# Optimization experiments

Hardware: AMD Instinct MI355X
Metric: run time of the kernel (lower is better)

The kernel has to match this reference:

```python
import jax, jax.numpy as jnp
import numpy as np

N_NODES = 50000
N_EDGES = 800000
N_GRAPHS = 128
F_IN = 36
HEADS1 = 10
OUT_DIM = 128


def _gat_layer(x, src, dst, W, a_src, a_dst, b, heads, out_c):
    # x: [N, Fin]; W: [Fin, heads*out_c]; a_src/a_dst: [heads, out_c]; b: [heads*out_c]
    N = x.shape[0]
    h = (x @ W).reshape(N, heads, out_c)                      # [N,H,C]
    al_s = jnp.einsum('nhc,hc->nh', h, a_src)                 # [N,H]
    al_d = jnp.einsum('nhc,hc->nh', h, a_dst)                 # [N,H]
    e = jax.nn.leaky_relu(al_s[src] + al_d[dst], negative_slope=0.2)  # [E,H]
    # segment-softmax over incoming edges of each dst node
    m = jax.ops.segment_max(e, dst, num_segments=N)
    m = jnp.where(jnp.isfinite(m), m, 0.0)
    p = jnp.exp(e - m[dst])
    s = jax.ops.segment_sum(p, dst, num_segments=N)
    alpha = p / (s[dst] + 1e-16)                              # [E,H]
    out = jax.ops.segment_sum(alpha[:, :, None] * h[src], dst, num_segments=N)  # [N,H,C]
    return out.reshape(N, heads * out_c) + b


def setup_inputs() -> dict:
    key = jax.random.key(0)
    ks = jax.random.split(key, 12)
    x = jax.random.normal(ks[0], (N_NODES, F_IN), dtype=jnp.float32)
    edge_index = jax.random.randint(ks[1], (2, N_EDGES), 0, N_NODES, dtype=jnp.int64)
    batch = jnp.sort(jax.random.randint(ks[2], (N_NODES,), 0, N_GRAPHS, dtype=jnp.int64))
    g = 0.1  # glorot-ish scale
    W1 = jax.random.normal(ks[3], (F_IN, HEADS1 * F_IN), dtype=jnp.float32) * g
    att_src1 = jax.random.normal(ks[4], (HEADS1, F_IN), dtype=jnp.float32) * g
    att_dst1 = jax.random.normal(ks[5], (HEADS1, F_IN), dtype=jnp.float32) * g
    b1 = jnp.zeros((HEADS1 * F_IN,), dtype=jnp.float32)
    W2 = jax.random.normal(ks[6], (HEADS1 * F_IN, OUT_DIM), dtype=jnp.float32) * g
    att_src2 = jax.random.normal(ks[7], (1, OUT_DIM), dtype=jnp.float32) * g
    att_dst2 = jax.random.normal(ks[8], (1, OUT_DIM), dtype=jnp.float32) * g
    b2 = jnp.zeros((OUT_DIM,), dtype=jnp.float32)
    fc_w = jax.random.normal(ks[9], (OUT_DIM, OUT_DIM), dtype=jnp.float32) * g
    fc_b = jnp.zeros((OUT_DIM,), dtype=jnp.float32)
    return {"x": x, "edge_index": edge_index, "batch": batch,
            "W1": W1, "att_src1": att_src1, "att_dst1": att_dst1, "b1": b1,
            "W2": W2, "att_src2": att_src2, "att_dst2": att_dst2, "b2": b2,
            "fc_w": fc_w, "fc_b": fc_b}


def reference(x, edge_index, batch, W1, att_src1, att_dst1, b1,
              W2, att_src2, att_dst2, b2, fc_w, fc_b):
    N = x.shape[0]
    # PyG GATConv adds self loops by default
    loops = jnp.arange(N, dtype=edge_index.dtype)
    src = jnp.concatenate([edge_index[0], loops])
    dst = jnp.concatenate([edge_index[1], loops])
    # eval mode: dropouts are identity
    h = jax.nn.elu(_gat_layer(x, src, dst, W1, att_src1, att_dst1, b1, HEADS1, F_IN))
    h = _gat_layer(h, src, dst, W2, att_src2, att_dst2, b2, 1, OUT_DIM)
    h = jax.nn.relu(h)
    # global max pool over graphs
    g = jax.ops.segment_max(h, batch, num_segments=N_GRAPHS)
    g = jnp.where(jnp.isfinite(g), g, 0.0)
    out = jax.nn.relu(g @ fc_w + fc_b)
    return out
```

## Files before the change

kernel.cpp:

```cpp
#include <hip/hip_runtime.h>
#include <hip/hip_fp16.h>
#include <math.h>

#define N_NODES  50000
#define N_EDGES  800000
#define E_TOT    850000
#define N_GRAPHS 128
#define F_IN     36
#define NH1      10
#define C1       36
#define D1       360
#define D2       128
#define XW       18

#define SCHUNK  512
#define NCHUNK  98

typedef unsigned int u32;

#if defined(__has_builtin)
#if __has_builtin(__builtin_amdgcn_fdot2)
#define HAVE_FDOT2 1
#endif
#endif
#ifndef HAVE_FDOT2
#define HAVE_FDOT2 0
#endif

typedef _Float16 h2v __attribute__((ext_vector_type(2)));

static __device__ __forceinline__ float2 h2f(u32 u) {
  __half2 h = __builtin_bit_cast(__half2, u);
  return __half22float2(h);
}
static __device__ __forceinline__ u32 f2h2(float a, float b) {
  __half2 h = __floats2half2_rn(a, b);
  return __builtin_bit_cast(u32, h);
}
static __device__ __forceinline__ float dot2acc(u32 a, u32 b, float acc) {
#if HAVE_FDOT2
  return __builtin_amdgcn_fdot2(__builtin_bit_cast(h2v, a), __builtin_bit_cast(h2v, b), acc, false);
#else
  float2 fa = h2f(a), fb = h2f(b);
  return fmaf(fa.x, fb.x, fmaf(fa.y, fb.y, acc));
#endif
}

__global__ void k_init(int* counts, u32* pool) {
  int i = blockIdx.x * blockDim.x + threadIdx.x;
  if (i < N_NODES) counts[i] = 0;
  if (i < N_GRAPHS * D2) pool[i] = 0u;
}

__global__ void k_hist(const int* ei, int* counts) {
  int e = blockIdx.x * blockDim.x + threadIdx.x;
  if (e >= E_TOT) return;
  int d = (e < N_EDGES) ? ei[N_EDGES + e] : (e - N_EDGES);
  atomicAdd(&counts[d], 1);
}

__global__ void k_scan1(const int* counts, int* partial) {
  __shared__ int red[256];
  int b = blockIdx.x, t = threadIdx.x;
  int base = b * SCHUNK;
  int v = 0;
  int i0 = base + t, i1 = base + t + 256;
  if (i0 < N_NODES) v += counts[i0];
  if (i1 < N_NODES) v += counts[i1];
  red[t] = v; __syncthreads();
  for (int off = 128; off; off >>= 1) {
    if (t < off) red[t] += red[t + off];
    __syncthreads();
  }
  if (t == 0) partial[b] = red[0];
}

__global__ void k_scan2(const int* partial, int* chunk_off, int* row_ptr) {
  if (threadIdx.x == 0 && blockIdx.x == 0) {
    int acc = 0;
    for (int i = 0; i < NCHUNK; i++) { chunk_off[i] = acc; acc += partial[i]; }
    row_ptr[N_NODES] = acc;
  }
}

__global__ void k_scan3(const int* counts, const int* chunk_off, int* row_ptr, int* nxt) {
  __shared__ int tmp[SCHUNK];
  int b = blockIdx.x, t = threadIdx.x;
  int i = b * SCHUNK + t;
  int v = (i < N_NODES) ? counts[i] : 0;
  tmp[t] = v; __syncthreads();
  for (int off = 1; off < SCHUNK; off <<= 1) {
    int x = (t >= off) ? tmp[t - off] : 0;
    __syncthreads();
    tmp[t] += x;
    __syncthreads();
  }
  if (i < N_NODES) {
    int excl = chunk_off[b] + tmp[t] - v;
    row_ptr[i] = excl;
    nxt[i] = excl;
  }
}

__global__ void k_scatter(const int* ei, int* nxt, int* csr_src) {
  int e = blockIdx.x * blockDim.x + threadIdx.x;
  if (e >= E_TOT) return;
  int s, d;
  if (e < N_EDGES) { s = ei[e]; d = ei[N_EDGES + e]; }
  else             { s = d = e - N_EDGES; }
  int pos = atomicAdd(&nxt[d], 1);
  csr_src[pos] = s;
}

__global__ void k_prep(const float* __restrict__ W1, const float* __restrict__ asrc,
                       const float* __restrict__ adst, const float* __restrict__ W2,
                       float* w_als, float* w_ald, u32* W1t2, u32* W2h) {
  int id = blockIdx.x * blockDim.x + threadIdx.x;
  if (id < D1) {
    int h = id / F_IN, k = id - h * F_IN;
    float sa = 0.f, sd = 0.f;
    for (int c = 0; c < C1; c++) {
      float wv = W1[k * D1 + h * C1 + c];
      sa = fmaf(wv, asrc[h * C1 + c], sa);
      sd = fmaf(wv, adst[h * C1 + c], sd);
    }
    w_als[id] = sa; w_ald[id] = sd;
  } else if (id < D1 + D1 * (F_IN / 2)) {
    int i = id - D1;
    int hc = i / (F_IN / 2), kp = i - hc * (F_IN / 2);
    W1t2[i] = f2h2(W1[(2 * kp) * D1 + hc], W1[(2 * kp + 1) * D1 + hc]);
  } else if (id < D1 + D1 * (F_IN / 2) + (D1 / 2) * D2) {
    int i = id - D1 - D1 * (F_IN / 2);
    int kp = i / D2, col = i - kp * D2;
    W2h[i] = f2h2(W2[(2 * kp) * D2 + col], W2[(2 * kp + 1) * D2 + col]);
  }
}

__global__ __launch_bounds__(256)
void k_als1(const float* __restrict__ x, const float* __restrict__ w_als,
            const float* __restrict__ w_ald, float* als, float* ald,
            u32* __restrict__ xh2) {
  __shared__ float xs[64][F_IN + 1];
  __shared__ float wa[D1], wd[D1];
  int t = threadIdx.x;
  int nb = blockIdx.x * 64;
  for (int i = t; i < D1; i += 256) { wa[i] = w_als[i]; wd[i] = w_ald[i]; }
  int lim = min(64, N_NODES - nb);
  for (int i = t; i < lim * F_IN; i += 256) {
    int n = i / F_IN, k = i - n * F_IN;
    xs[n][k] = x[(size_t)(nb + n) * F_IN + k];
  }
  __syncthreads();
  for (int i = t; i < lim * XW; i += 256) {
    int n = i / XW, kp = i - n * XW;
    xh2[(size_t)(nb + n) * XW + kp] = f2h2(xs[n][2 * kp], xs[n][2 * kp + 1]);
  }
  for (int pair = t; pair < lim * NH1; pair += 256) {
    int n = pair / NH1, h = pair - n * NH1;
    const float* xp = xs[n];
    const float* wap = &wa[h * F_IN];
    const float* wdp = &wd[h * F_IN];
    float sa = 0.f, sd = 0.f;
#pragma unroll
    for (int k = 0; k < F_IN; k++) {
      float xv = xp[k];
      sa = fmaf(xv, wap[k], sa);
      sd = fmaf(xv, wdp[k], sd);
    }
    als[(size_t)(nb + n) * NH1 + h] = sa;
    ald[(size_t)(nb + n) * NH1 + h] = sd;
  }
}

__global__ __launch_bounds__(256)
void k_agg1(const u32* __restrict__ xrow, const float* __restrict__ als,
            const float* __restrict__ ald, const int* __restrict__ row_ptr,
            const int* __restrict__ csr_src, u32* __restrict__ aggx2) {
  __shared__ float pl[4][64][NH1];
  int w = threadIdx.x >> 6, lane = threadIdx.x & 63;
  int node = blockIdx.x * 4 + w;
  int beg = row_ptr[node], end = row_ptr[node + 1];

  int h0 = lane / XW,  kp0 = lane - XW * h0;
  int s1 = lane + 64;
  int h1i = s1 / XW,   kp1 = s1 - XW * h1i;
  bool v2 = lane < 52;
  int s2 = v2 ? lane + 128 : 179;
  int h2i = s2 / XW,   kp2 = s2 - XW * h2i;

  float aldn[NH1];
#pragma unroll
  for (int h = 0; h < NH1; h++) aldn[h] = ald[(size_t)node * NH1 + h];
  float a0x = 0.f, a0y = 0.f, a1x = 0.f, a1y = 0.f, a2x = 0.f, a2y = 0.f;
  float sp[NH1];
#pragma unroll
  for (int h = 0; h < NH1; h++) sp[h] = 0.f;

  for (int base = beg; base < end; base += 64) {
    int cnt = min(64, end - base);
    float p[NH1];
    int msrc = 0;
    if (lane < cnt) {
      msrc = csr_src[base + lane];
      const float2* ap = (const float2*)(als + (size_t)msrc * NH1);
#pragma unroll
      for (int q = 0; q < 5; q++) {
        float2 v = ap[q];
        float v0 = v.x + aldn[2 * q];
        float v1 = v.y + aldn[2 * q + 1];
        v0 = v0 > 0.f ? v0 : 0.2f * v0;
        v1 = v1 > 0.f ? v1 : 0.2f * v1;
        p[2 * q] = __expf(v0);
        p[2 * q + 1] = __expf(v1);
      }
    } else {
#pragma unroll
      for (int h = 0; h < NH1; h++) p[h] = 0.f;
    }
#pragma unroll
    for (int h = 0; h < NH1; h++) sp[h] += p[h];
    float2* plw = (float2*)pl[w][lane];
#pragma unroll
    for (int q = 0; q < 5; q++) plw[q] = float2{p[2 * q], p[2 * q + 1]};
    __builtin_amdgcn_wave_barrier();

    int j2 = 0;
    for (; j2 + 2 <= cnt; j2 += 2) {
      int sA = __shfl(msrc, j2), sB = __shfl(msrc, j2 + 1);
      const u32* ra = xrow + (size_t)sA * XW;
      const u32* rb = xrow + (size_t)sB * XW;
      u32 ua0 = ra[kp0], ua1 = ra[kp1], ua2 = ra[kp2];
      u32 ub0 = rb[kp0], ub1 = rb[kp1], ub2 = rb[kp2];
      const float* pA = pl[w][j2];
      const float* pB = pl[w][j2 + 1];
      float cA0 = pA[h0], cA1 = pA[h1i], cA2 = pA[h2i];
      float cB0 = pB[h0], cB1 = pB[h1i], cB2 = pB[h2i];
      float2 f;
      f = h2f(ua0); a0x = fmaf(cA0, f.x, a0x); a0y = fmaf(cA0, f.y, a0y);
      f = h2f(ua1); a1x = fmaf(cA1, f.x, a1x); a1y = fmaf(cA1, f.y, a1y);
      f = h2f(ua2); a2x = fmaf(cA2, f.x, a2x); a2y = fmaf(cA2, f.y, a2y);
      f = h2f(ub0); a0x = fmaf(cB0, f.x, a0x); a0y = fmaf(cB0, f.y, a0y);
      f = h2f(ub1); a1x = fmaf(cB1, f.x, a1x); a1y = fmaf(cB1, f.y, a1y);
      f = h2f(ub2); a2x = fmaf(cB2, f.x, a2x); a2y = fmaf(cB2, f.y, a2y);
    }
    if (j2 < cnt) {
      int sA = __shfl(msrc, j2);
      const u32* ra = xrow + (size_t)sA * XW;
      u32 ua0 = ra[kp0], ua1 = ra[kp1], ua2 = ra[kp2];
      const float* pA = pl[w][j2];
      float cA0 = pA[h0], cA1 = pA[h1i], cA2 = pA[h2i];
      float2 f;
      f = h2f(ua0); a0x = fmaf(cA0, f.x, a0x); a0y = fmaf(cA0, f.y, a0y);
      f = h2f(ua1); a1x = fmaf(cA1, f.x, a1x); a1y = fmaf(cA1, f.y, a1y);
      f = h2f(ua2); a2x = fmaf(cA2, f.x, a2x); a2y = fmaf(cA2, f.y, a2y);
    }
    __builtin_amdgcn_wave_barrier();
  }

#pragma unroll
  for (int h = 0; h < NH1; h++) {
    float t = sp[h];
#pragma unroll
    for (int off = 32; off; off >>= 1) t += __shfl_xor(t, off);
    sp[h] = t;
  }
  float i0 = 1.f / (sp[h0] + 1e-16f);
  float i1 = 1.f / (sp[h1i] + 1e-16f);
  float i2 = 1.f / (sp[h2i] + 1e-16f);
  u32* orow = aggx2 + (size_t)node * (D1 / 2);
  orow[lane] = f2h2(a0x * i0, a0y * i0);
  orow[lane + 64] = f2h2(a1x * i1, a1y * i1);
  if (v2) orow[lane + 128] = f2h2(a2x * i2, a2y * i2);
}

#define MIX_NPB 32
__global__ __launch_bounds__(384)
void k_mix1(const u32* __restrict__ aggx2, const u32* __restrict__ W1t2,
            const float* __restrict__ b1, __half* __restrict__ hact) {
  __shared__ u32 ag[MIX_NPB][D1 / 2 + 4];
  int t = threadIdx.x;
  int nb = blockIdx.x * MIX_NPB;
  int lim = min(MIX_NPB, N_NODES - nb);
  const u32* gsrc = aggx2 + (size_t)nb * (D1 / 2);
  for (int i = t; i < lim * (D1 / 2); i += 384) {
    int n = i / (D1 / 2), k = i - n * (D1 / 2);
    ag[n][k] = gsrc[i];
  }
  __syncthreads();
  if (t < D1) {
    int h = t / C1;
    u32 wreg[F_IN / 2];
#pragma unroll
    for (int kp = 0; kp < F_IN / 2; kp++) wreg[kp] = W1t2[t * (F_IN / 2) + kp];
    float bj = b1[t];
    for (int n = 0; n < lim; n++) {
      const u32* a = &ag[n][h * (F_IN / 2)];
      float acc2 = 0.f;
#pragma unroll
      for (int kp = 0; kp < F_IN / 2; kp++) acc2 = dot2acc(a[kp], wreg[kp], acc2);
      float val = acc2 + bj;
      val = val > 0.f ? val : __expf(val) - 1.f;
      hact[(size_t)(nb + n) * D1 + t] = __float2half(val);
    }
  }
}

#define G2_NPB 16
__global__ __launch_bounds__(256)
void k_gemm2(const __half* __restrict__ hacth, const u32* __restrict__ W2h,
             __half* __restrict__ h2h) {
  __shared__ u32 hs2[D1 / 2][G2_NPB];
  int nb = blockIdx.x * G2_NPB;
  int t = threadIdx.x;
  for (int i = t; i < G2_NPB * (D1 / 2); i += 256) {
    int n = i / (D1 / 2), kp = i - n * (D1 / 2);
    hs2[kp][n] = ((const u32*)(hacth + (size_t)(nb + n) * D1))[kp];
  }
  __syncthreads();
  int col = t & 127, ng = t >> 7;
  float acc[8];
#pragma unroll
  for (int i = 0; i < 8; i++) acc[i] = 0.f;
#pragma unroll 2
  for (int kp = 0; kp < D1 / 2; kp++) {
    u32 wv = W2h[kp * D2 + col];
    uint4 r0 = *(const uint4*)&hs2[kp][ng * 8];
    uint4 r1 = *(const uint4*)&hs2[kp][ng * 8 + 4];
    acc[0] = dot2acc(r0.x, wv, acc[0]);
    acc[1] = dot2acc(r0.y, wv, acc[1]);
    acc[2] = dot2acc(r0.z, wv, acc[2]);
    acc[3] = dot2acc(r0.w, wv, acc[3]);
    acc[4] = dot2acc(r1.x, wv, acc[4]);
    acc[5] = dot2acc(r1.y, wv, acc[5]);
    acc[6] = dot2acc(r1.z, wv, acc[6]);
    acc[7] = dot2acc(r1.w, wv, acc[7]);
  }
#pragma unroll
  for (int i = 0; i < 8; i++)
    h2h[(size_t)(nb + ng * 8 + i) * D2 + col] = __float2half(acc[i]);
}

__global__ void k_als2(const __half* __restrict__ h2h, const float* __restrict__ asrc,
                       const float* __restrict__ adst, float* als, float* ald) {
  int node = blockIdx.x * 4 + (threadIdx.x >> 6);
  int lane = threadIdx.x & 63;
  const u32* hr = (const u32*)(h2h + (size_t)node * D2);
  float2 f = h2f(hr[lane]);
  float2 a = ((const float2*)asrc)[lane];
  float2 d = ((const float2*)adst)[lane];
  float ps = f.x * a.x + f.y * a.y;
  float pd = f.x * d.x + f.y * d.y;
#pragma unroll
  for (int off = 32; off; off >>= 1) { ps += __shfl_xor(ps, off); pd += __shfl_xor(pd, off); }
  if (lane == 0) { als[node] = ps; ald[node] = pd; }
}

__global__ __launch_bounds__(256)
void k_agg2(const __half* __restrict__ h2h, const float* __restrict__ als,
            const float* __restrict__ ald, const int* __restrict__ row_ptr,
            const int* __restrict__ csr_src, const float* __restrict__ b2,
            const int* __restrict__ batch, u32* __restrict__ pool) {
  int w = threadIdx.x >> 6, lane = threadIdx.x & 63;
  int node = blockIdx.x * 4 + w;
  int beg = row_ptr[node], end = row_ptr[node + 1];
  float aldn = ald[node];
  float ax = 0.f, ay = 0.f, ssum = 0.f;
  for (int base = beg; base < end; base += 64) {
    int cnt = min(64, end - base);
    int msrc = 0; float p = 0.f;
    if (lane < cnt) {
      msrc = csr_src[base + lane];
      float vv = als[msrc] + aldn;
      vv = vv > 0.f ? vv : 0.2f * vv;
      p = __expf(vv);
    }
    ssum += p;
    int j2 = 0;
    for (; j2 + 2 <= cnt; j2 += 2) {
      int sA = __shfl(msrc, j2), sB = __shfl(msrc, j2 + 1);
      float cA = __shfl(p, j2), cB = __shfl(p, j2 + 1);
      u32 ua = ((const u32*)(h2h + (size_t)sA * D2))[lane];
      u32 ub = ((const u32*)(h2h + (size_t)sB * D2))[lane];
      float2 f = h2f(ua); ax = fmaf(cA, f.x, ax); ay = fmaf(cA, f.y, ay);
      f = h2f(ub); ax = fmaf(cB, f.x, ax); ay = fmaf(cB, f.y, ay);
    }
    if (j2 < cnt) {
      int sA = __shfl(msrc, j2);
      float cA = __shfl(p, j2);
      u32 ua = ((const u32*)(h2h + (size_t)sA * D2))[lane];
      float2 f = h2f(ua); ax = fmaf(cA, f.x, ax); ay = fmaf(cA, f.y, ay);
    }
  }
  float t2 = ssum;
#pragma unroll
  for (int off = 32; off; off >>= 1) t2 += __shfl_xor(t2, off);
  float inv = 1.f / (t2 + 1e-16f);
  float2 bv = ((const float2*)b2)[lane];
  float vx = fmaxf(ax * inv + bv.x, 0.f);
  float vy = fmaxf(ay * inv + bv.y, 0.f);
  int g = batch[node];
  atomicMax(&pool[g * D2 + 2 * lane], __float_as_uint(vx));
  atomicMax(&pool[g * D2 + 2 * lane + 1], __float_as_uint(vy));
}

__global__ void k_final(const float* __restrict__ pool, const float* __restrict__ fcw,
                        const float* __restrict__ fcb, float* __restrict__ out) {
  __shared__ float ps[D2];
  int g = blockIdx.x, j = threadIdx.x;
  ps[j] = pool[g * D2 + j];
  __syncthreads();
  float acc = 0.f;
  for (int c = 0; c < D2; c++) acc = fmaf(ps[c], fcw[c * D2 + j], acc);
  acc += fcb[j];
  out[g * D2 + j] = acc > 0.f ? acc : 0.f;
}

extern "C" void kernel_launch(void* const* d_in, const int* in_sizes, int n_in,
                              void* d_out, int out_size, void* d_ws, size_t ws_size,
                              hipStream_t stream) {
  const float* x     = (const float*)d_in[0];
  const int*   ei    = (const int*)d_in[1];
  const int*   batch = (const int*)d_in[2];
  const float* W1    = (const float*)d_in[3];
  const float* asrc1 = (const float*)d_in[4];
  const float* adst1 = (const float*)d_in[5];
  const float* b1    = (const float*)d_in[6];
  const float* W2    = (const float*)d_in[7];
  const float* asrc2 = (const float*)d_in[8];
  const float* adst2 = (const float*)d_in[9];
  const float* b2    = (const float*)d_in[10];
  const float* fcw   = (const float*)d_in[11];
  const float* fcb   = (const float*)d_in[12];
  float* out = (float*)d_out;

  char* w = (char*)d_ws;
  size_t off = 0;
  auto alloc = [&](size_t bytes) -> char* {
    char* p = w + off;
    off = (off + bytes + 255) & ~(size_t)255;
    return p;
  };
  int* counts    = (int*)alloc((size_t)N_NODES * 4);
  int* row_ptr   = (int*)alloc((size_t)(N_NODES + 1) * 4);
  int* nxt       = (int*)alloc((size_t)N_NODES * 4);
  int* csr_src   = (int*)alloc((size_t)E_TOT * 4);
  int* partial   = (int*)alloc(NCHUNK * 4);
  int* chunk_off = (int*)alloc(NCHUNK * 4);
  float* als1    = (float*)alloc((size_t)N_NODES * NH1 * 4);
  float* ald1    = (float*)alloc((size_t)N_NODES * NH1 * 4);
  float* als2    = (float*)alloc((size_t)N_NODES * 4);
  float* ald2    = (float*)alloc((size_t)N_NODES * 4);
  u32*   pool    = (u32*)alloc((size_t)N_GRAPHS * D2 * 4);
  float* w_als   = (float*)alloc((size_t)D1 * 4);
  float* w_ald   = (float*)alloc((size_t)D1 * 4);
  u32*   W1t2    = (u32*)alloc((size_t)D1 * (F_IN / 2) * 4);
  u32*   W2h     = (u32*)alloc((size_t)(D1 / 2) * D2 * 4);
  u32*   xh2     = (u32*)alloc((size_t)N_NODES * XW * 4);
  u32*   aggx2   = (u32*)alloc((size_t)N_NODES * (D1 / 2) * 4);
  __half* hacth  = (__half*)alloc((size_t)N_NODES * D1 * 2);
  __half* h2h    = (__half*)alloc((size_t)N_NODES * D2 * 2);

  k_init<<<dim3(196), dim3(256), 0, stream>>>(counts, pool);
  k_hist<<<dim3((E_TOT + 255) / 256), dim3(256), 0, stream>>>(ei, counts);
  k_scan1<<<dim3(NCHUNK), dim3(256), 0, stream>>>(counts, partial);
  k_scan2<<<dim3(1), dim3(64), 0, stream>>>(partial, chunk_off, row_ptr);
  k_scan3<<<dim3(NCHUNK), dim3(SCHUNK), 0, stream>>>(counts, chunk_off, row_ptr, nxt);
  k_scatter<<<dim3((E_TOT + 255) / 256), dim3(256), 0, stream>>>(ei, nxt, csr_src);
  k_prep<<<dim3(117), dim3(256), 0, stream>>>(W1, asrc1, adst1, W2, w_als, w_ald, W1t2, W2h);

  k_als1<<<dim3((N_NODES + 63) / 64), dim3(256), 0, stream>>>(x, w_als, w_ald, als1, ald1, xh2);
  k_agg1<<<dim3(N_NODES / 4), dim3(256), 0, stream>>>(xh2, als1, ald1, row_ptr, csr_src, aggx2);
  k_mix1<<<dim3((N_NODES + MIX_NPB - 1) / MIX_NPB), dim3(384), 0, stream>>>(aggx2, W1t2, b1, hacth);

  k_gemm2<<<dim3(N_NODES / G2_NPB), dim3(256), 0, stream>>>(hacth, W2h, h2h);
  k_als2<<<dim3(N_NODES / 4), dim3(256), 0, stream>>>(h2h, asrc2, adst2, als2, ald2);
  k_agg2<<<dim3(N_NODES / 4), dim3(256), 0, stream>>>(h2h, als2, ald2, row_ptr, csr_src,
                                                      b2, batch, pool);

  k_final<<<dim3(N_GRAPHS), dim3(D2), 0, stream>>>((const float*)pool, fcw, fcb, out);

  (void)in_sizes; (void)n_in; (void)out_size; (void)ws_size;
}
```

Before: 481.2 us.

## Use MFMA for layer-2 GEMM, unroll agg1 by four, filter pool atomics

Rewrites the layer-2 dense transform to use MFMA 16x16x16 f16 instructions, reading activations from a 384-wide padded layout and a W2 matrix pre-swizzled into MFMA fragment order. This replaces the dot2-based shared-memory GEMM. The layer-1 edge gather loop is unrolled from two to four neighbours to get more loads in flight. Pool atomicMax calls are skipped when a plain read shows the current value is already larger, and the h2 buffer now reuses the aggx2 workspace. The padding adds zero-fill writes in mix1, and the unsynchronized pre-read before each atomic is only a hint.

```diff
diff --git a/kernel.cpp b/kernel.cpp
--- a/kernel.cpp
+++ b/kernel.cpp
@@ -12,6 +12,10 @@
 #define D1       360
 #define D2       128
 #define XW       18
+#define HPAD     384
+#define KW       192
+#define KCH      24
+#define W2FW     24576
 
 #define SCHUNK  512
 #define NCHUNK  98
@@ -28,6 +32,8 @@
 #endif
 
 typedef _Float16 h2v __attribute__((ext_vector_type(2)));
+typedef _Float16 f16x4 __attribute__((ext_vector_type(4)));
+typedef float f32x4 __attribute__((ext_vector_type(4)));
 
 static __device__ __forceinline__ float2 h2f(u32 u) {
   __half2 h = __builtin_bit_cast(__half2, u);
@@ -114,7 +120,7 @@
 
 __global__ void k_prep(const float* __restrict__ W1, const float* __restrict__ asrc,
                        const float* __restrict__ adst, const float* __restrict__ W2,
-                       float* w_als, float* w_ald, u32* W1t2, u32* W2h) {
+                       float* w_als, float* w_ald, u32* W1t2, u32* W2f) {
   int id = blockIdx.x * blockDim.x + threadIdx.x;
   if (id < D1) {
     int h = id / F_IN, k = id - h * F_IN;
@@ -129,10 +135,18 @@
     int i = id - D1;
     int hc = i / (F_IN / 2), kp = i - hc * (F_IN / 2);
     W1t2[i] = f2h2(W1[(2 * kp) * D1 + hc], W1[(2 * kp + 1) * D1 + hc]);
-  } else if (id < D1 + D1 * (F_IN / 2) + (D1 / 2) * D2) {
+  } else if (id < D1 + D1 * (F_IN / 2) + W2FW) {
     int i = id - D1 - D1 * (F_IN / 2);
-    int kp = i / D2, col = i - kp * D2;
-    W2h[i] = f2h2(W2[(2 * kp) * D2 + col], W2[(2 * kp + 1) * D2 + col]);
+    int q    = i & 1;
+    int lane = (i >> 1) & 63;
+    int rem  = i >> 7;
+    int t    = rem & 7;
+    int kc   = rem >> 3;
+    int k0   = kc * 16 + ((lane >> 4) << 2) + 2 * q;
+    int col  = t * 16 + (lane & 15);
+    float w0 = (k0     < D1) ? W2[(size_t)k0 * D2 + col]       : 0.f;
+    float w1 = (k0 + 1 < D1) ? W2[(size_t)(k0 + 1) * D2 + col] : 0.f;
+    W2f[i] = f2h2(w0, w1);
   }
 }
 
@@ -225,16 +239,25 @@
     __builtin_amdgcn_wave_barrier();
 
     int j2 = 0;
-    for (; j2 + 2 <= cnt; j2 += 2) {
-      int sA = __shfl(msrc, j2), sB = __shfl(msrc, j2 + 1);
+    for (; j2 + 4 <= cnt; j2 += 4) {
+      int sA = __shfl(msrc, j2),     sB = __shfl(msrc, j2 + 1);
+      int sC = __shfl(msrc, j2 + 2), sD = __shfl(msrc, j2 + 3);
       const u32* ra = xrow + (size_t)sA * XW;
       const u32* rb = xrow + (size_t)sB * XW;
+      const u32* rc = xrow + (size_t)sC * XW;
+      const u32* rd = xrow + (size_t)sD * XW;
       u32 ua0 = ra[kp0], ua1 = ra[kp1], ua2 = ra[kp2];
       u32 ub0 = rb[kp0], ub1 = rb[kp1], ub2 = rb[kp2];
+      u32 uc0 = rc[kp0], uc1 = rc[kp1], uc2 = rc[kp2];
+      u32 ud0 = rd[kp0], ud1 = rd[kp1], ud2 = rd[kp2];
       const float* pA = pl[w][j2];
       const float* pB = pl[w][j2 + 1];
+      const float* pC = pl[w][j2 + 2];
+      const float* pD = pl[w][j2 + 3];
       float cA0 = pA[h0], cA1 = pA[h1i], cA2 = pA[h2i];
       float cB0 = pB[h0], cB1 = pB[h1i], cB2 = pB[h2i];
+      float cC0 = pC[h0], cC1 = pC[h1i], cC2 = pC[h2i];
+      float cD0 = pD[h0], cD1 = pD[h1i], cD2 = pD[h2i];
       float2 f;
       f = h2f(ua0); a0x = fmaf(cA0, f.x, a0x); a0y = fmaf(cA0, f.y, a0y);
       f = h2f(ua1); a1x = fmaf(cA1, f.x, a1x); a1y = fmaf(cA1, f.y, a1y);
@@ -242,8 +265,14 @@
       f = h2f(ub0); a0x = fmaf(cB0, f.x, a0x); a0y = fmaf(cB0, f.y, a0y);
       f = h2f(ub1); a1x = fmaf(cB1, f.x, a1x); a1y = fmaf(cB1, f.y, a1y);
       f = h2f(ub2); a2x = fmaf(cB2, f.x, a2x); a2y = fmaf(cB2, f.y, a2y);
-    }
-    if (j2 < cnt) {
+      f = h2f(uc0); a0x = fmaf(cC0, f.x, a0x); a0y = fmaf(cC0, f.y, a0y);
+      f = h2f(uc1); a1x = fmaf(cC1, f.x, a1x); a1y = fmaf(cC1, f.y, a1y);
+      f = h2f(uc2); a2x = fmaf(cC2, f.x, a2x); a2y = fmaf(cC2, f.y, a2y);
+      f = h2f(ud0); a0x = fmaf(cD0, f.x, a0x); a0y = fmaf(cD0, f.y, a0y);
+      f = h2f(ud1); a1x = fmaf(cD1, f.x, a1x); a1y = fmaf(cD1, f.y, a1y);
+      f = h2f(ud2); a2x = fmaf(cD2, f.x, a2x); a2y = fmaf(cD2, f.y, a2y);
+    }
+    for (; j2 < cnt; j2++) {
       int sA = __shfl(msrc, j2);
       const u32* ra = xrow + (size_t)sA * XW;
       u32 ua0 = ra[kp0], ua1 = ra[kp1], ua2 = ra[kp2];
@@ -300,44 +329,49 @@
       for (int kp = 0; kp < F_IN / 2; kp++) acc2 = dot2acc(a[kp], wreg[kp], acc2);
       float val = acc2 + bj;
       val = val > 0.f ? val : __expf(val) - 1.f;
-      hact[(size_t)(nb + n) * D1 + t] = __float2half(val);
-    }
-  }
-}
-
-#define G2_NPB 16
+      hact[(size_t)(nb + n) * HPAD + t] = __float2half(val);
+    }
+  } else {
+    for (int n = 0; n < lim; n++)
+      hact[(size_t)(nb + n) * HPAD + t] = __float2half(0.f);
+  }
+}
+
 __global__ __launch_bounds__(256)
-void k_gemm2(const __half* __restrict__ hacth, const u32* __restrict__ W2h,
+void k_gemm2(const u32* __restrict__ hact32, const u32* __restrict__ W2f,
              __half* __restrict__ h2h) {
-  __shared__ u32 hs2[D1 / 2][G2_NPB];
-  int nb = blockIdx.x * G2_NPB;
-  int t = threadIdx.x;
-  for (int i = t; i < G2_NPB * (D1 / 2); i += 256) {
-    int n = i / (D1 / 2), kp = i - n * (D1 / 2);
-    hs2[kp][n] = ((const u32*)(hacth + (size_t)(nb + n) * D1))[kp];
-  }
-  __syncthreads();
-  int col = t & 127, ng = t >> 7;
-  float acc[8];
-#pragma unroll
-  for (int i = 0; i < 8; i++) acc[i] = 0.f;
-#pragma unroll 2
-  for (int kp = 0; kp < D1 / 2; kp++) {
-    u32 wv = W2h[kp * D2 + col];
-    uint4 r0 = *(const uint4*)&hs2[kp][ng * 8];
-    uint4 r1 = *(const uint4*)&hs2[kp][ng * 8 + 4];
-    acc[0] = dot2acc(r0.x, wv, acc[0]);
-    acc[1] = dot2acc(r0.y, wv, acc[1]);
-    acc[2] = dot2acc(r0.z, wv, acc[2]);
-    acc[3] = dot2acc(r0.w, wv, acc[3]);
-    acc[4] = dot2acc(r1.x, wv, acc[4]);
-    acc[5] = dot2acc(r1.y, wv, acc[5]);
-    acc[6] = dot2acc(r1.z, wv, acc[6]);
-    acc[7] = dot2acc(r1.w, wv, acc[7]);
-  }
-#pragma unroll
-  for (int i = 0; i < 8; i++)
-    h2h[(size_t)(nb + ng * 8 + i) * D2 + col] = __float2half(acc[i]);
+  int w = threadIdx.x >> 6, l = threadIdx.x & 63;
+  int rowbase = blockIdx.x * 64 + w * 16;
+  int m = l & 15, kb = l >> 4;
+  int arow = rowbase + m;
+  if (arow >= N_NODES) arow = N_NODES - 1;
+  const u32* ap = hact32 + (size_t)arow * KW + kb * 2;
+  const uint2* bp = (const uint2*)W2f;
+  f32x4 acc[8];
+#pragma unroll
+  for (int t = 0; t < 8; t++) acc[t] = (f32x4){0.f, 0.f, 0.f, 0.f};
+#pragma unroll 4
+  for (int kc = 0; kc < KCH; kc++) {
+    uint2 aw = *(const uint2*)(ap + kc * 8);
+    f16x4 af = __builtin_bit_cast(f16x4, aw);
+#pragma unroll
+    for (int t = 0; t < 8; t++) {
+      uint2 bw = bp[(kc * 8 + t) * 64 + l];
+      acc[t] = __builtin_amdgcn_mfma_f32_16x16x16f16(af, __builtin_bit_cast(f16x4, bw),
+                                                     acc[t], 0, 0, 0);
+    }
+  }
+  int orow0 = rowbase + (l >> 4) * 4;
+  int col0 = l & 15;
+#pragma unroll
+  for (int t = 0; t < 8; t++) {
+#pragma unroll
+    for (int r = 0; r < 4; r++) {
+      int row = orow0 + r;
+      if (row < N_NODES)
+        h2h[(size_t)row * D2 + t * 16 + col0] = __float2half(acc[t][r]);
+    }
+  }
 }
 
 __global__ void k_als2(const __half* __restrict__ h2h, const float* __restrict__ asrc,
@@ -399,8 +433,10 @@
   float vx = fmaxf(ax * inv + bv.x, 0.f);
   float vy = fmaxf(ay * inv + bv.y, 0.f);
   int g = batch[node];
-  atomicMax(&pool[g * D2 + 2 * lane], __float_as_uint(vx));
-  atomicMax(&pool[g * D2 + 2 * lane + 1], __float_as_uint(vy));
+  u32 bx = __float_as_uint(vx), by = __float_as_uint(vy);
+  u32* p0 = pool + (size_t)g * D2 + 2 * lane;
+  if (bx > p0[0]) atomicMax(&p0[0], bx);
+  if (by > p0[1]) atomicMax(&p0[1], by);
 }
 
 __global__ void k_final(const float* __restrict__ pool, const float* __restrict__ fcw,
@@ -454,11 +490,11 @@
   float* w_als   = (float*)alloc((size_t)D1 * 4);
   float* w_ald   = (float*)alloc((size_t)D1 * 4);
   u32*   W1t2    = (u32*)alloc((size_t)D1 * (F_IN / 2) * 4);
-  u32*   W2h     = (u32*)alloc((size_t)(D1 / 2) * D2 * 4);
+  u32*   W2f     = (u32*)alloc((size_t)W2FW * 4);
   u32*   xh2     = (u32*)alloc((size_t)N_NODES * XW * 4);
   u32*   aggx2   = (u32*)alloc((size_t)N_NODES * (D1 / 2) * 4);
-  __half* hacth  = (__half*)alloc((size_t)N_NODES * D1 * 2);
-  __half* h2h    = (__half*)alloc((size_t)N_NODES * D2 * 2);
+  __half* hacth  = (__half*)alloc((size_t)N_NODES * HPAD * 2);
+  __half* h2h = (__half*)aggx2;
 
   k_init<<<dim3(196), dim3(256), 0, stream>>>(counts, pool);
   k_hist<<<dim3((E_TOT + 255) / 256), dim3(256), 0, stream>>>(ei, counts);
@@ -466,13 +502,13 @@
   k_scan2<<<dim3(1), dim3(64), 0, stream>>>(partial, chunk_off, row_ptr);
   k_scan3<<<dim3(NCHUNK), dim3(SCHUNK), 0, stream>>>(counts, chunk_off, row_ptr, nxt);
   k_scatter<<<dim3((E_TOT + 255) / 256), dim3(256), 0, stream>>>(ei, nxt, csr_src);
-  k_prep<<<dim3(117), dim3(256), 0, stream>>>(W1, asrc1, adst1, W2, w_als, w_ald, W1t2, W2h);
+  k_prep<<<dim3(123), dim3(256), 0, stream>>>(W1, asrc1, adst1, W2, w_als, w_ald, W1t2, W2f);
 
   k_als1<<<dim3((N_NODES + 63) / 64), dim3(256), 0, stream>>>(x, w_als, w_ald, als1, ald1, xh2);
   k_agg1<<<dim3(N_NODES / 4), dim3(256), 0, stream>>>(xh2, als1, ald1, row_ptr, csr_src, aggx2);
   k_mix1<<<dim3((N_NODES + MIX_NPB - 1) / MIX_NPB), dim3(384), 0, stream>>>(aggx2, W1t2, b1, hacth);
 
-  k_gemm2<<<dim3(N_NODES / G2_NPB), dim3(256), 0, stream>>>(hacth, W2h, h2h);
+  k_gemm2<<<dim3((N_NODES + 63) / 64), dim3(256), 0, stream>>>((const u32*)hacth, W2f, h2h);
   k_als2<<<dim3(N_NODES / 4), dim3(256), 0, stream>>>(h2h, asrc2, adst2, als2, ald2);
   k_agg2<<<dim3(N_NODES / 4), dim3(256), 0, stream>>>(h2h, als2, ald2, row_ptr, csr_src,
                                                       b2, batch, pool);
```

Measured after the change: 551.9 us. 14.7% more time.
